# Performance work log

Measured on AMD Instinct MI355X. Metric: run time of the kernel, lower is better.

Reference implementation:

```python
import jax, jax.numpy as jnp
import numpy as np

B, T, D, K = 4, 4096, 1024, 64


def setup_inputs() -> dict:
    key = jax.random.key(0)
    k1, k2, k3, k4 = jax.random.split(key, 4)
    x = jax.random.normal(k1, (B, T, D), dtype=jnp.float32)
    Wq = jax.random.normal(k2, (D, K), dtype=jnp.float32) * (D ** -0.5)
    Wk = jax.random.normal(k3, (D, K), dtype=jnp.float32) * (D ** -0.5)
    Wv = jax.random.normal(k4, (D, D), dtype=jnp.float32) * (D ** -0.5)
    return {"x": x, "Wq": Wq, "Wk": Wk, "Wv": Wv}


def reference(x, Wq, Wk, Wv):
    # x: (B,T,D); single-head causal self-attention with value dim = D
    Bx, Tx, Dx = x.shape
    head_size = Wq.shape[-1]
    q = jnp.einsum('btd,dk->btk', x, Wq)  # (B,T,K)
    k = jnp.einsum('btd,dk->btk', x, Wk)  # (B,T,K)
    v = jnp.einsum('btd,de->bte', x, Wv)  # (B,T,D)
    scores = jnp.einsum('bqk,bsk->bqs', q, k) * (head_size ** -0.5)  # (B,T,T)
    causal = jnp.tril(jnp.ones((Tx, Tx), dtype=bool))
    scores = jnp.where(causal[None, :, :], scores, -jnp.inf)
    attn = jax.nn.softmax(scores, axis=-1)
    return jnp.einsum('bqs,bsd->bqd', attn, v)  # (B,T,D)
```

## Files before the change

kernel.cpp:

```cpp
#include <hip/hip_runtime.h>
#include <hip/hip_bf16.h>

typedef __attribute__((ext_vector_type(8))) short bf16x8;
typedef __attribute__((ext_vector_type(4))) float f32x4;
typedef unsigned short u16;

#define MFMA16(a, b, c) __builtin_amdgcn_mfma_f32_16x16x32_bf16((a), (b), (c), 0, 0, 0)
#define GLLDS(gp, lp)                                                                  \
  __builtin_amdgcn_global_load_lds((const __attribute__((address_space(1))) unsigned int*)(gp), \
                                   (__attribute__((address_space(3))) unsigned int*)(lp), 16, 0, 0)

__device__ __forceinline__ u16 f2b(float f) {
  union { float f; unsigned u; } x; x.f = f;
  return (u16)((x.u + 0x7FFFu + ((x.u >> 16) & 1u)) >> 16);
}
__device__ __forceinline__ u16 f2b_hw(float f) {
  union { __hip_bfloat16 h; u16 u; } c;
  c.h = __float2bfloat16(f);
  return c.u;
}

__global__ __launch_bounds__(256) void k_cvt(const float* __restrict__ in,
                                             u16* __restrict__ out, int n4) {
  int i = blockIdx.x * 256 + threadIdx.x;
  if (i >= n4) return;
  float4 v = ((const float4*)in)[i];
  u16 a = f2b(v.x), b = f2b(v.y), c = f2b(v.z), d = f2b(v.w);
  ((uint2*)out)[i] = make_uint2((unsigned)a | ((unsigned)b << 16),
                                (unsigned)c | ((unsigned)d << 16));
}

__global__ __launch_bounds__(256) void k_packT(const float* __restrict__ in,
                                               u16* __restrict__ out, int R, int C) {
  __shared__ float t[32][33];
  int r0 = blockIdx.x * 32, c0 = blockIdx.y * 32;
  int cx = threadIdx.x & 31, ry = threadIdx.x >> 5;
#pragma unroll
  for (int k = 0; k < 4; k++)
    t[ry + k * 8][cx] = in[(size_t)(r0 + ry + k * 8) * C + c0 + cx];
  __syncthreads();
#pragma unroll
  for (int k = 0; k < 4; k++)
    out[(size_t)(c0 + ry + k * 8) * R + r0 + cx] = f2b(t[cx][ry + k * 8]);
}

__global__ __launch_bounds__(256) void k_gemm_qk(const u16* __restrict__ xb,
                                                 const u16* __restrict__ wqt,
                                                 const u16* __restrict__ wkt,
                                                 u16* __restrict__ q, u16* __restrict__ kk) {
  int row0 = blockIdx.x * 64;
  int tid = threadIdx.x, w = tid >> 6, l = tid & 63, l15 = l & 15, lg = l >> 4;
  const u16* wt = (w < 2) ? wqt : wkt;
  int nbase = (w & 1) * 32;
  f32x4 acc[4][2];
#pragma unroll
  for (int mt = 0; mt < 4; mt++)
#pragma unroll
    for (int nt = 0; nt < 2; nt++) acc[mt][nt] = (f32x4){0.f, 0.f, 0.f, 0.f};

  for (int k0 = 0; k0 < 1024; k0 += 32) {
    bf16x8 bfr[2], afr[4];
#pragma unroll
    for (int nt = 0; nt < 2; nt++)
      bfr[nt] = *(const bf16x8*)&wt[(size_t)(nbase + nt * 16 + l15) * 1024 + k0 + lg * 8];
#pragma unroll
    for (int mt = 0; mt < 4; mt++)
      afr[mt] = *(const bf16x8*)&xb[(size_t)(row0 + mt * 16 + l15) * 1024 + k0 + lg * 8];
#pragma unroll
    for (int mt = 0; mt < 4; mt++)
#pragma unroll
      for (int nt = 0; nt < 2; nt++) acc[mt][nt] = MFMA16(afr[mt], bfr[nt], acc[mt][nt]);
  }
  if (w < 2) {
#pragma unroll
    for (int mt = 0; mt < 4; mt++)
#pragma unroll
      for (int nt = 0; nt < 2; nt++)
#pragma unroll
        for (int j = 0; j < 4; j++)
          q[(size_t)(row0 + mt * 16 + lg * 4 + j) * 64 + nbase + nt * 16 + l15] =
              f2b(acc[mt][nt][j] * 0.125f);
  } else {
#pragma unroll
    for (int mt = 0; mt < 4; mt++)
#pragma unroll
      for (int nt = 0; nt < 2; nt++)
#pragma unroll
        for (int j = 0; j < 4; j++) {
          int row = row0 + mt * 16 + lg * 4 + j;
          int c = (nbase + nt * 16 + l15) * 2;
          size_t off = (size_t)(row >> 6) * 8192 + (row & 63) * 128 + (c ^ ((row & 7) << 4));
          *(u16*)((char*)kk + off) = f2b(acc[mt][nt][j]);
        }
  }
}

__global__ __launch_bounds__(256) void k_gemm_v(const u16* __restrict__ xb,
                                                const u16* __restrict__ wvt,
                                                u16* __restrict__ vT) {
  int b = blockIdx.z;
  int d0 = blockIdx.y * 128;
  int s0 = blockIdx.x * 128;
  int tid = threadIdx.x, w = tid >> 6, l = tid & 63, l15 = l & 15, lg = l >> 4;
  int wd = (w & 1) * 64, wsn = (w >> 1) * 64;
  __shared__ __align__(16) char lds[32768];

  const u16* arow = wvt + (size_t)d0 * 1024;
  const u16* brow = xb + (size_t)(b * 4096 + s0) * 1024;

  auto stage = [&](int buf, int k0) {
    char* La = lds + buf * 16384;
    char* Lb = La + 8192;
#pragma unroll
    for (int i = 0; i < 2; i++) {
      int row = w * 32 + i * 16 + (l >> 2), kq = (l & 3) * 8;
      GLLDS(&arow[(size_t)row * 1024 + k0 + kq], La + (w * 2 + i) * 1024);
      GLLDS(&brow[(size_t)row * 1024 + k0 + kq], Lb + (w * 2 + i) * 1024);
    }
  };

  f32x4 acc[4][4];
#pragma unroll
  for (int mt = 0; mt < 4; mt++)
#pragma unroll
    for (int nt = 0; nt < 4; nt++) acc[mt][nt] = (f32x4){0.f, 0.f, 0.f, 0.f};

  stage(0, 0);
  __syncthreads();
  int buf = 0;
  for (int k = 0; k < 32; k++) {
    if (k < 31) stage(buf ^ 1, (k + 1) * 32);
    const char* La = lds + buf * 16384;
    const char* Lb = La + 8192;
    bf16x8 afr[4], bfr[4];
#pragma unroll
    for (int mt = 0; mt < 4; mt++)
      afr[mt] = *(const bf16x8*)(La + (wd + mt * 16 + l15) * 64 + lg * 16);
#pragma unroll
    for (int nt = 0; nt < 4; nt++)
      bfr[nt] = *(const bf16x8*)(Lb + (wsn + nt * 16 + l15) * 64 + lg * 16);
    __builtin_amdgcn_s_setprio(1);
#pragma unroll
    for (int mt = 0; mt < 4; mt++)
#pragma unroll
      for (int nt = 0; nt < 4; nt++) acc[mt][nt] = MFMA16(afr[mt], bfr[nt], acc[mt][nt]);
    __builtin_amdgcn_s_setprio(0);
    __syncthreads();
    buf ^= 1;
  }
#pragma unroll
  for (int mt = 0; mt < 4; mt++)
#pragma unroll
    for (int nt = 0; nt < 4; nt++)
#pragma unroll
      for (int j = 0; j < 4; j++) {
        int d = d0 + wd + mt * 16 + lg * 4 + j;
        int s = s0 + wsn + nt * 16 + l15;
        size_t off = ((size_t)(b * 64 + (s >> 6)) * 8 + (d >> 7)) * 16384 + (d & 127) * 128 +
                     (((s & 63) * 2) ^ ((d & 7) << 4));
        *(u16*)((char*)vT + off) = f2b(acc[mt][nt][j]);
      }
}

__global__ __launch_bounds__(512, 2) void k_attn(const u16* __restrict__ qw,
                                                 const u16* __restrict__ kws,
                                                 const u16* __restrict__ vts,
                                                 float* __restrict__ out) {
  int p = blockIdx.x, cpair = blockIdx.y, b = blockIdx.z;
  int tid = threadIdx.x, w = tid >> 6, l = tid & 63, l15 = l & 15, lg = l >> 4;
  int sw = (l15 & 7) << 4;
  size_t tokb = (size_t)b * 4096;

  __shared__ __align__(16) char lds[98816];
  char* Pb = lds + 81920;
  float* scb = (float*)(lds + 98304);

  const short ob = (short)0x3F80;
  const bf16x8 ones = {ob, ob, ob, ob, ob, ob, ob, ob};

  auto stage = [&](int t, int bufi) {
    const char* kb = (const char*)kws + (size_t)(b * 64 + t) * 8192;
    const char* vb = (const char*)vts + ((size_t)(b * 64 + t) * 8 + cpair * 2) * 16384;
    char* lk = lds + bufi * 8192;
    char* lv = lds + 16384 + bufi * 32768;
#pragma unroll
    for (int i = 0; i < 5; i++) {
      int s = w * 5 + i;
      if (s < 8) GLLDS(kb + s * 1024 + l * 16, lk + s * 1024);
      else       GLLDS(vb + (s - 8) * 1024 + l * 16, lv + (s - 8) * 1024);
    }
  };

  auto run_phase = [&](int Q0) {
    int ntb = (Q0 >> 6) + 2;
    int qsA = Q0 + w * 16;
    int qA = qsA + l15;
    int qsB = Q0 + (w & 3) * 32;
    int dhalf = w >> 2;

    bf16x8 qf[2];
#pragma unroll
    for (int ks = 0; ks < 2; ks++)
      qf[ks] = *(const bf16x8*)&qw[(tokb + qA) * 64 + ks * 32 + lg * 8];

    f32x4 acc[8][2], accl[2];
    float mrow = -1e30f;
#pragma unroll
    for (int mt = 0; mt < 8; mt++)
#pragma unroll
      for (int qt = 0; qt < 2; qt++) acc[mt][qt] = (f32x4){0.f, 0.f, 0.f, 0.f};
    accl[0] = (f32x4){0.f, 0.f, 0.f, 0.f};
    accl[1] = (f32x4){0.f, 0.f, 0.f, 0.f};

    stage(0, 0);
    __syncthreads();
    int buf = 0;
    for (int t = 0; t < ntb; t++) {
      int s0 = t * 64;
      if (t + 1 < ntb) stage(t + 1, buf ^ 1);
      if (s0 < qsA + 16) {
        const char* Kb = lds + buf * 8192;
        f32x4 sfr[4];
        __builtin_amdgcn_s_setprio(1);
#pragma unroll
        for (int nt = 0; nt < 4; nt++) {
          const char* kr = Kb + (nt * 16 + l15) * 128;
          bf16x8 kf0 = *(const bf16x8*)(kr + ((lg * 16) ^ sw));
          bf16x8 kf1 = *(const bf16x8*)(kr + ((64 + lg * 16) ^ sw));
          f32x4 z = (f32x4){0.f, 0.f, 0.f, 0.f};
          z = MFMA16(kf0, qf[0], z);
          sfr[nt] = MFMA16(kf1, qf[1], z);
        }
        __builtin_amdgcn_s_setprio(0);
        if (s0 + 63 > qsA) {
#pragma unroll
          for (int nt = 0; nt < 4; nt++)
#pragma unroll
            for (int j = 0; j < 4; j++)
              if (s0 + nt * 16 + lg * 4 + j > qA) sfr[nt][j] = -1e30f;
        }
        float pm = fmaxf(fmaxf(fmaxf(sfr[0][0], sfr[0][1]), fmaxf(sfr[0][2], sfr[0][3])),
                         fmaxf(fmaxf(sfr[1][0], sfr[1][1]), fmaxf(sfr[1][2], sfr[1][3])));
        pm = fmaxf(pm, fmaxf(fmaxf(fmaxf(sfr[2][0], sfr[2][1]), fmaxf(sfr[2][2], sfr[2][3])),
                             fmaxf(fmaxf(sfr[3][0], sfr[3][1]), fmaxf(sfr[3][2], sfr[3][3]))));
        pm = fmaxf(pm, __shfl_xor(pm, 16));
        pm = fmaxf(pm, __shfl_xor(pm, 32));
        float sc = 1.0f;
        if (__any(pm > mrow + 8.0f)) {
          float mn = fmaxf(mrow, pm);
          sc = __expf(mrow - mn);
          mrow = mn;
        }
        int rq = w * 16 + l15;
        scb[rq] = sc;
        int rbase = rq * 128, sx = (rq & 7) << 4;
#pragma unroll
        for (int nt = 0; nt < 4; nt++) {
          unsigned lo = (unsigned)f2b_hw(__expf(sfr[nt][0] - mrow)) |
                        ((unsigned)f2b_hw(__expf(sfr[nt][1] - mrow)) << 16);
          unsigned hi = (unsigned)f2b_hw(__expf(sfr[nt][2] - mrow)) |
                        ((unsigned)f2b_hw(__expf(sfr[nt][3] - mrow)) << 16);
          int addr = (rbase + (nt * 16 + lg * 4) * 2) ^ sx;
          *(uint2*)(Pb + addr) = make_uint2(lo, hi);
        }
      }
      __syncthreads();
      const char* Vb = lds + 16384 + buf * 32768 + dhalf * 16384;
#pragma unroll
      for (int qt = 0; qt < 2; qt++) {
        if (s0 < qsB + qt * 16 + 16) {
          float sq = scb[(w & 3) * 32 + qt * 16 + l15];
          if (!__all(sq == 1.0f)) {
#pragma unroll
            for (int mt = 0; mt < 8; mt++) acc[mt][qt] *= sq;
            accl[qt] *= sq;
          }
          int R = (w & 3) * 32 + qt * 16 + l15;
          int rx = (R & 7) << 4;
          bf16x8 pf0 = *(const bf16x8*)(Pb + ((R * 128 + lg * 16) ^ rx));
          bf16x8 pf1 = *(const bf16x8*)(Pb + ((R * 128 + 64 + lg * 16) ^ rx));
          __builtin_amdgcn_s_setprio(1);
          accl[qt] = MFMA16(ones, pf0, accl[qt]);
          accl[qt] = MFMA16(ones, pf1, accl[qt]);
#pragma unroll
          for (int mt = 0; mt < 8; mt++) {
            const char* vr = Vb + (mt * 16 + l15) * 128;
            bf16x8 va0 = *(const bf16x8*)(vr + ((lg * 16) ^ sw));
            bf16x8 va1 = *(const bf16x8*)(vr + ((64 + lg * 16) ^ sw));
            acc[mt][qt] = MFMA16(va0, pf0, acc[mt][qt]);
            acc[mt][qt] = MFMA16(va1, pf1, acc[mt][qt]);
          }
          __builtin_amdgcn_s_setprio(0);
        }
      }
      __syncthreads();
      buf ^= 1;
    }
#pragma unroll
    for (int qt = 0; qt < 2; qt++) {
      float linv = 1.0f / accl[qt][0];
#pragma unroll
      for (int mt = 0; mt < 8; mt++) {
        f32x4 v = acc[mt][qt] * linv;
        size_t o = (tokb + qsB + qt * 16 + l15) * 1024 + cpair * 256 + dhalf * 128 +
                   mt * 16 + lg * 4;
        *(f32x4*)&out[o] = v;
      }
    }
  };

  run_phase(p * 128);
  run_phase((31 - p) * 128);
}

extern "C" void kernel_launch(void* const* d_in, const int* in_sizes, int n_in,
                              void* d_out, int out_size, void* d_ws, size_t ws_size,
                              hipStream_t stream) {
  const float* x  = (const float*)d_in[0];
  const float* Wq = (const float*)d_in[1];
  const float* Wk = (const float*)d_in[2];
  const float* Wv = (const float*)d_in[3];
  float* out = (float*)d_out;
  char* ws = (char*)d_ws;
  u16* xb  = (u16*)(ws);
  u16* qw  = (u16*)(ws + 33554432);
  u16* kw  = (u16*)(ws + 35651584);
  u16* vT  = (u16*)(ws + 37748736);
  u16* wqt = (u16*)(ws + 71303168);
  u16* wkt = (u16*)(ws + 71434240);
  u16* wvt = (u16*)(ws + 71565312);

  k_cvt<<<16384, 256, 0, stream>>>(x, xb, 4194304);
  k_packT<<<dim3(32, 2), 256, 0, stream>>>(Wq, wqt, 1024, 64);
  k_packT<<<dim3(32, 2), 256, 0, stream>>>(Wk, wkt, 1024, 64);
  k_packT<<<dim3(32, 32), 256, 0, stream>>>(Wv, wvt, 1024, 1024);
  k_gemm_qk<<<256, 256, 0, stream>>>(xb, wqt, wkt, qw, kw);
  k_gemm_v<<<dim3(32, 8, 4), 256, 0, stream>>>(xb, wvt, vT);
  k_attn<<<dim3(16, 4, 4), 512, 0, stream>>>(qw, kw, vT, out);
}
```

Measured before the change: 237.5 us.

## Merge PV query-tile loops to share V fragments and use finer-grained barriers

The two query sub-tiles of the PV stage are now processed together. Each V fragment loaded from LDS feeds both accumulators, which halves V LDS reads, and an inactive first sub-tile is handled by zeroed P fragments instead of a branch. The full __syncthreads calls are replaced with explicit s_waitcnt plus s_barrier: only LDS counters are waited on mid-iteration, and global loads are drained only at the end of each iteration. The change risks extra MFMAs on masked diagonal tiles and depends on the hand-placed waitcnt being correct for the global_load_lds async copies.

```diff
diff --git a/kernel.cpp b/kernel.cpp
--- a/kernel.cpp
+++ b/kernel.cpp
@@ -177,6 +177,7 @@
 
   const short ob = (short)0x3F80;
   const bf16x8 ones = {ob, ob, ob, ob, ob, ob, ob, ob};
+  const bf16x8 zf = {0, 0, 0, 0, 0, 0, 0, 0};
 
   auto stage = [&](int t, int bufi) {
     const char* kb = (const char*)kws + (size_t)(b * 64 + t) * 8192;
@@ -213,7 +214,9 @@
     accl[1] = (f32x4){0.f, 0.f, 0.f, 0.f};
 
     stage(0, 0);
-    __syncthreads();
+    asm volatile("s_waitcnt vmcnt(0)" ::: "memory");
+    __builtin_amdgcn_s_barrier();
+    asm volatile("" ::: "memory");
     int buf = 0;
     for (int t = 0; t < ntb; t++) {
       int s0 = t * 64;
@@ -264,36 +267,60 @@
           *(uint2*)(Pb + addr) = make_uint2(lo, hi);
         }
       }
-      __syncthreads();
-      const char* Vb = lds + 16384 + buf * 32768 + dhalf * 16384;
-#pragma unroll
-      for (int qt = 0; qt < 2; qt++) {
-        if (s0 < qsB + qt * 16 + 16) {
-          float sq = scb[(w & 3) * 32 + qt * 16 + l15];
-          if (!__all(sq == 1.0f)) {
-#pragma unroll
-            for (int mt = 0; mt < 8; mt++) acc[mt][qt] *= sq;
-            accl[qt] *= sq;
+      asm volatile("s_waitcnt lgkmcnt(0)" ::: "memory");
+      __builtin_amdgcn_s_barrier();
+      asm volatile("" ::: "memory");
+      if (s0 < qsB + 32) {
+        const char* Vb = lds + 16384 + buf * 32768 + dhalf * 16384;
+        bool act0 = s0 < qsB + 16;
+        int R0 = (w & 3) * 32 + l15;
+        if (act0) {
+          float sq0 = scb[R0];
+          if (!__all(sq0 == 1.0f)) {
+#pragma unroll
+            for (int mt = 0; mt < 8; mt++) acc[mt][0] *= sq0;
+            accl[0] *= sq0;
           }
-          int R = (w & 3) * 32 + qt * 16 + l15;
-          int rx = (R & 7) << 4;
-          bf16x8 pf0 = *(const bf16x8*)(Pb + ((R * 128 + lg * 16) ^ rx));
-          bf16x8 pf1 = *(const bf16x8*)(Pb + ((R * 128 + 64 + lg * 16) ^ rx));
-          __builtin_amdgcn_s_setprio(1);
-          accl[qt] = MFMA16(ones, pf0, accl[qt]);
-          accl[qt] = MFMA16(ones, pf1, accl[qt]);
-#pragma unroll
-          for (int mt = 0; mt < 8; mt++) {
-            const char* vr = Vb + (mt * 16 + l15) * 128;
-            bf16x8 va0 = *(const bf16x8*)(vr + ((lg * 16) ^ sw));
-            bf16x8 va1 = *(const bf16x8*)(vr + ((64 + lg * 16) ^ sw));
-            acc[mt][qt] = MFMA16(va0, pf0, acc[mt][qt]);
-            acc[mt][qt] = MFMA16(va1, pf1, acc[mt][qt]);
+        }
+        {
+          float sq1 = scb[R0 + 16];
+          if (!__all(sq1 == 1.0f)) {
+#pragma unroll
+            for (int mt = 0; mt < 8; mt++) acc[mt][1] *= sq1;
+            accl[1] *= sq1;
           }
-          __builtin_amdgcn_s_setprio(0);
-        }
+        }
+        bf16x8 pf00 = zf, pf01 = zf, pf10, pf11;
+        if (act0) {
+          int rx = (R0 & 7) << 4;
+          pf00 = *(const bf16x8*)(Pb + ((R0 * 128 + lg * 16) ^ rx));
+          pf01 = *(const bf16x8*)(Pb + ((R0 * 128 + 64 + lg * 16) ^ rx));
+        }
+        {
+          int R1 = R0 + 16, rx = (R1 & 7) << 4;
+          pf10 = *(const bf16x8*)(Pb + ((R1 * 128 + lg * 16) ^ rx));
+          pf11 = *(const bf16x8*)(Pb + ((R1 * 128 + 64 + lg * 16) ^ rx));
+        }
+        __builtin_amdgcn_s_setprio(1);
+        accl[0] = MFMA16(ones, pf00, accl[0]);
+        accl[0] = MFMA16(ones, pf01, accl[0]);
+        accl[1] = MFMA16(ones, pf10, accl[1]);
+        accl[1] = MFMA16(ones, pf11, accl[1]);
+#pragma unroll
+        for (int mt = 0; mt < 8; mt++) {
+          const char* vr = Vb + (mt * 16 + l15) * 128;
+          bf16x8 va0 = *(const bf16x8*)(vr + ((lg * 16) ^ sw));
+          bf16x8 va1 = *(const bf16x8*)(vr + ((64 + lg * 16) ^ sw));
+          acc[mt][0] = MFMA16(va0, pf00, acc[mt][0]);
+          acc[mt][0] = MFMA16(va1, pf01, acc[mt][0]);
+          acc[mt][1] = MFMA16(va0, pf10, acc[mt][1]);
+          acc[mt][1] = MFMA16(va1, pf11, acc[mt][1]);
+        }
+        __builtin_amdgcn_s_setprio(0);
       }
-      __syncthreads();
+      asm volatile("s_waitcnt vmcnt(0)" ::: "memory");
+      __builtin_amdgcn_s_barrier();
+      asm volatile("" ::: "memory");
       buf ^= 1;
     }
 #pragma unroll
```

After: 252.6 us. 6.3% more time.

## Warp-specialize attention: score warps feed PV warps via double-buffered P

Applied to the files above, without the earlier changes.

Splits the eight waves of the attention block into four producer waves that compute QK scores, softmax and write P, and four consumer waves that run P·V one tile behind, using a double-buffered P and scale buffer in LDS. This lets the QK and softmax stage overlap the PV MFMA stage instead of serialising them within every wave. Each consumer wave now holds 4x8 accumulators, which raises register pressure. The grid is also flattened and remapped so blocks sharing a batch and column pair land on the same XCD for L2 reuse, and K and V staging is split across waves.

```diff
diff --git a/kernel.cpp b/kernel.cpp
--- a/kernel.cpp
+++ b/kernel.cpp
@@ -14,10 +14,10 @@
   union { float f; unsigned u; } x; x.f = f;
   return (u16)((x.u + 0x7FFFu + ((x.u >> 16) & 1u)) >> 16);
 }
-__device__ __forceinline__ u16 f2b_hw(float f) {
+__device__ __forceinline__ unsigned f2b_hw(float f) {
   union { __hip_bfloat16 h; u16 u; } c;
   c.h = __float2bfloat16(f);
-  return c.u;
+  return (unsigned)c.u;
 }
 
 __global__ __launch_bounds__(256) void k_cvt(const float* __restrict__ in,
@@ -166,145 +166,196 @@
                                                  const u16* __restrict__ kws,
                                                  const u16* __restrict__ vts,
                                                  float* __restrict__ out) {
-  int p = blockIdx.x, cpair = blockIdx.y, b = blockIdx.z;
+  int bid = blockIdx.x;
+  int xcd = bid & 7, rest = bid >> 3;
+  int p = rest & 15, hi = rest >> 4;
+  int g = xcd + 8 * hi;
+  int cpair = g & 3, b = g >> 2;
   int tid = threadIdx.x, w = tid >> 6, l = tid & 63, l15 = l & 15, lg = l >> 4;
   int sw = (l15 & 7) << 4;
   size_t tokb = (size_t)b * 4096;
-
-  __shared__ __align__(16) char lds[98816];
-  char* Pb = lds + 81920;
-  float* scb = (float*)(lds + 98304);
+  bool isA = w < 4;
+  int wq = w & 3;
+  int qpos = wq & 1, dhalf = wq >> 1;
+
+  __shared__ __align__(16) char lds[115712];
 
   const short ob = (short)0x3F80;
   const bf16x8 ones = {ob, ob, ob, ob, ob, ob, ob, ob};
 
-  auto stage = [&](int t, int bufi) {
+  auto stageV = [&](int t, int bufi) {
+    const char* vb = (const char*)vts + ((size_t)(b * 64 + t) * 8 + cpair * 2) * 16384;
+    char* lv = lds + 16384 + bufi * 32768;
+#pragma unroll
+    for (int i = 0; i < 4; i++) GLLDS(vb + (w * 4 + i) * 1024 + l * 16, lv + (w * 4 + i) * 1024);
+  };
+  auto stageK = [&](int t, int bufi) {
     const char* kb = (const char*)kws + (size_t)(b * 64 + t) * 8192;
-    const char* vb = (const char*)vts + ((size_t)(b * 64 + t) * 8 + cpair * 2) * 16384;
-    char* lk = lds + bufi * 8192;
-    char* lv = lds + 16384 + bufi * 32768;
-#pragma unroll
-    for (int i = 0; i < 5; i++) {
-      int s = w * 5 + i;
-      if (s < 8) GLLDS(kb + s * 1024 + l * 16, lk + s * 1024);
-      else       GLLDS(vb + (s - 8) * 1024 + l * 16, lv + (s - 8) * 1024);
-    }
+    GLLDS(kb + w * 1024 + l * 16, lds + bufi * 8192 + w * 1024);
   };
 
   auto run_phase = [&](int Q0) {
     int ntb = (Q0 >> 6) + 2;
-    int qsA = Q0 + w * 16;
-    int qA = qsA + l15;
-    int qsB = Q0 + (w & 3) * 32;
-    int dhalf = w >> 2;
-
-    bf16x8 qf[2];
-#pragma unroll
-    for (int ks = 0; ks < 2; ks++)
-      qf[ks] = *(const bf16x8*)&qw[(tokb + qA) * 64 + ks * 32 + lg * 8];
-
-    f32x4 acc[8][2], accl[2];
-    float mrow = -1e30f;
+    int qsA = Q0 + wq * 32;
+    int qsB = Q0 + qpos * 64;
+
+    bf16x8 qf[2][2];
+    if (isA) {
+#pragma unroll
+      for (int cb = 0; cb < 2; cb++)
+#pragma unroll
+        for (int ks = 0; ks < 2; ks++)
+          qf[cb][ks] =
+              *(const bf16x8*)&qw[(tokb + qsA + cb * 16 + l15) * 64 + ks * 32 + lg * 8];
+    }
+
+    f32x4 acc[8][4], accl[4];
+    float mrow[2];
 #pragma unroll
     for (int mt = 0; mt < 8; mt++)
 #pragma unroll
-      for (int qt = 0; qt < 2; qt++) acc[mt][qt] = (f32x4){0.f, 0.f, 0.f, 0.f};
-    accl[0] = (f32x4){0.f, 0.f, 0.f, 0.f};
-    accl[1] = (f32x4){0.f, 0.f, 0.f, 0.f};
-
-    stage(0, 0);
+      for (int qt = 0; qt < 4; qt++) acc[mt][qt] = (f32x4){0.f, 0.f, 0.f, 0.f};
+#pragma unroll
+    for (int qt = 0; qt < 4; qt++) accl[qt] = (f32x4){0.f, 0.f, 0.f, 0.f};
+    mrow[0] = mrow[1] = -1e30f;
+
+    stageK(0, 0);
     __syncthreads();
-    int buf = 0;
-    for (int t = 0; t < ntb; t++) {
-      int s0 = t * 64;
-      if (t + 1 < ntb) stage(t + 1, buf ^ 1);
-      if (s0 < qsA + 16) {
-        const char* Kb = lds + buf * 8192;
-        f32x4 sfr[4];
-        __builtin_amdgcn_s_setprio(1);
-#pragma unroll
-        for (int nt = 0; nt < 4; nt++) {
-          const char* kr = Kb + (nt * 16 + l15) * 128;
-          bf16x8 kf0 = *(const bf16x8*)(kr + ((lg * 16) ^ sw));
-          bf16x8 kf1 = *(const bf16x8*)(kr + ((64 + lg * 16) ^ sw));
-          f32x4 z = (f32x4){0.f, 0.f, 0.f, 0.f};
-          z = MFMA16(kf0, qf[0], z);
-          sfr[nt] = MFMA16(kf1, qf[1], z);
+    for (int t = 0; t <= ntb; t++) {
+      if (t < ntb) stageV(t, t & 1);
+      if (t + 1 < ntb) stageK(t + 1, (t + 1) & 1);
+      if (isA) {
+        int s0 = t * 64;
+        if (t < ntb && s0 < qsA + 32) {
+          const char* Kb = lds + (t & 1) * 8192;
+          char* Pw = lds + 81920 + (t & 1) * 16384;
+          float* scw = (float*)(lds + 114688) + (t & 1) * 128;
+          f32x4 sfr[2][4];
+          __builtin_amdgcn_s_setprio(1);
+#pragma unroll
+          for (int nt = 0; nt < 4; nt++) {
+            const char* kr = Kb + (nt * 16 + l15) * 128;
+            bf16x8 kf0 = *(const bf16x8*)(kr + ((lg * 16) ^ sw));
+            bf16x8 kf1 = *(const bf16x8*)(kr + ((64 + lg * 16) ^ sw));
+#pragma unroll
+            for (int cb = 0; cb < 2; cb++) {
+              f32x4 z = (f32x4){0.f, 0.f, 0.f, 0.f};
+              z = MFMA16(kf0, qf[cb][0], z);
+              sfr[cb][nt] = MFMA16(kf1, qf[cb][1], z);
+            }
+          }
+          __builtin_amdgcn_s_setprio(0);
+          if (s0 + 63 > qsA) {
+#pragma unroll
+            for (int cb = 0; cb < 2; cb++) {
+              int qv = qsA + cb * 16 + l15;
+#pragma unroll
+              for (int nt = 0; nt < 4; nt++)
+#pragma unroll
+                for (int j = 0; j < 4; j++)
+                  if (s0 + nt * 16 + lg * 4 + j > qv) sfr[cb][nt][j] = -1e30f;
+            }
+          }
+          float pm[2];
+          int need = 0;
+#pragma unroll
+          for (int cb = 0; cb < 2; cb++) {
+            pm[cb] = fmaxf(fmaxf(fmaxf(sfr[cb][0][0], sfr[cb][0][1]),
+                                 fmaxf(sfr[cb][0][2], sfr[cb][0][3])),
+                           fmaxf(fmaxf(sfr[cb][1][0], sfr[cb][1][1]),
+                                 fmaxf(sfr[cb][1][2], sfr[cb][1][3])));
+            pm[cb] = fmaxf(pm[cb], fmaxf(fmaxf(fmaxf(sfr[cb][2][0], sfr[cb][2][1]),
+                                               fmaxf(sfr[cb][2][2], sfr[cb][2][3])),
+                                         fmaxf(fmaxf(sfr[cb][3][0], sfr[cb][3][1]),
+                                               fmaxf(sfr[cb][3][2], sfr[cb][3][3]))));
+            pm[cb] = fmaxf(pm[cb], __shfl_xor(pm[cb], 16));
+            pm[cb] = fmaxf(pm[cb], __shfl_xor(pm[cb], 32));
+            need |= (pm[cb] > mrow[cb] + 8.0f);
+          }
+          float scv[2] = {1.0f, 1.0f};
+          if (__any(need)) {
+#pragma unroll
+            for (int cb = 0; cb < 2; cb++) {
+              float mn = fmaxf(mrow[cb], pm[cb]);
+              scv[cb] = __expf(mrow[cb] - mn);
+              mrow[cb] = mn;
+            }
+          }
+#pragma unroll
+          for (int cb = 0; cb < 2; cb++) {
+            int rq = wq * 32 + cb * 16 + l15;
+            scw[rq] = scv[cb];
+            int rbase = rq * 128, sx = (rq & 7) << 4;
+#pragma unroll
+            for (int nt = 0; nt < 4; nt++) {
+              unsigned lo = f2b_hw(__expf(sfr[cb][nt][0] - mrow[cb])) |
+                            (f2b_hw(__expf(sfr[cb][nt][1] - mrow[cb])) << 16);
+              unsigned hi2 = f2b_hw(__expf(sfr[cb][nt][2] - mrow[cb])) |
+                             (f2b_hw(__expf(sfr[cb][nt][3] - mrow[cb])) << 16);
+              int addr = (rbase + (nt * 16 + lg * 4) * 2) ^ sx;
+              *(uint2*)(Pw + addr) = make_uint2(lo, hi2);
+            }
+          }
         }
-        __builtin_amdgcn_s_setprio(0);
-        if (s0 + 63 > qsA) {
-#pragma unroll
-          for (int nt = 0; nt < 4; nt++)
-#pragma unroll
-            for (int j = 0; j < 4; j++)
-              if (s0 + nt * 16 + lg * 4 + j > qA) sfr[nt][j] = -1e30f;
-        }
-        float pm = fmaxf(fmaxf(fmaxf(sfr[0][0], sfr[0][1]), fmaxf(sfr[0][2], sfr[0][3])),
-                         fmaxf(fmaxf(sfr[1][0], sfr[1][1]), fmaxf(sfr[1][2], sfr[1][3])));
-        pm = fmaxf(pm, fmaxf(fmaxf(fmaxf(sfr[2][0], sfr[2][1]), fmaxf(sfr[2][2], sfr[2][3])),
-                             fmaxf(fmaxf(sfr[3][0], sfr[3][1]), fmaxf(sfr[3][2], sfr[3][3]))));
-        pm = fmaxf(pm, __shfl_xor(pm, 16));
-        pm = fmaxf(pm, __shfl_xor(pm, 32));
-        float sc = 1.0f;
-        if (__any(pm > mrow + 8.0f)) {
-          float mn = fmaxf(mrow, pm);
-          sc = __expf(mrow - mn);
-          mrow = mn;
-        }
-        int rq = w * 16 + l15;
-        scb[rq] = sc;
-        int rbase = rq * 128, sx = (rq & 7) << 4;
-#pragma unroll
-        for (int nt = 0; nt < 4; nt++) {
-          unsigned lo = (unsigned)f2b_hw(__expf(sfr[nt][0] - mrow)) |
-                        ((unsigned)f2b_hw(__expf(sfr[nt][1] - mrow)) << 16);
-          unsigned hi = (unsigned)f2b_hw(__expf(sfr[nt][2] - mrow)) |
-                        ((unsigned)f2b_hw(__expf(sfr[nt][3] - mrow)) << 16);
-          int addr = (rbase + (nt * 16 + lg * 4) * 2) ^ sx;
-          *(uint2*)(Pb + addr) = make_uint2(lo, hi);
-        }
-      }
-      __syncthreads();
-      const char* Vb = lds + 16384 + buf * 32768 + dhalf * 16384;
-#pragma unroll
-      for (int qt = 0; qt < 2; qt++) {
-        if (s0 < qsB + qt * 16 + 16) {
-          float sq = scb[(w & 3) * 32 + qt * 16 + l15];
-          if (!__all(sq == 1.0f)) {
-#pragma unroll
-            for (int mt = 0; mt < 8; mt++) acc[mt][qt] *= sq;
-            accl[qt] *= sq;
-          }
-          int R = (w & 3) * 32 + qt * 16 + l15;
-          int rx = (R & 7) << 4;
-          bf16x8 pf0 = *(const bf16x8*)(Pb + ((R * 128 + lg * 16) ^ rx));
-          bf16x8 pf1 = *(const bf16x8*)(Pb + ((R * 128 + 64 + lg * 16) ^ rx));
+      } else if (t >= 1) {
+        int tb = t - 1, s0 = tb * 64;
+        int qlo = (s0 - qsB) >> 4;
+        if (qlo < 0) qlo = 0;
+        if (qlo < 4) {
+          int bi = tb & 1;
+          const char* Pb = lds + 81920 + bi * 16384;
+          const float* scb = (const float*)(lds + 114688) + bi * 128;
+          const char* Vb = lds + 16384 + bi * 32768 + dhalf * 16384;
+          bf16x8 pf[4][2];
+#pragma unroll
+          for (int qt = 0; qt < 4; qt++)
+            if (qt >= qlo) {
+              int R = qpos * 64 + qt * 16 + l15;
+              float sq = scb[R];
+              if (!__all(sq == 1.0f)) {
+#pragma unroll
+                for (int mt = 0; mt < 8; mt++) acc[mt][qt] *= sq;
+                accl[qt] *= sq;
+              }
+              int rx = (R & 7) << 4;
+              pf[qt][0] = *(const bf16x8*)(Pb + ((R * 128 + lg * 16) ^ rx));
+              pf[qt][1] = *(const bf16x8*)(Pb + ((R * 128 + 64 + lg * 16) ^ rx));
+            }
           __builtin_amdgcn_s_setprio(1);
-          accl[qt] = MFMA16(ones, pf0, accl[qt]);
-          accl[qt] = MFMA16(ones, pf1, accl[qt]);
+#pragma unroll
+          for (int qt = 0; qt < 4; qt++)
+            if (qt >= qlo) {
+              accl[qt] = MFMA16(ones, pf[qt][0], accl[qt]);
+              accl[qt] = MFMA16(ones, pf[qt][1], accl[qt]);
+            }
 #pragma unroll
           for (int mt = 0; mt < 8; mt++) {
             const char* vr = Vb + (mt * 16 + l15) * 128;
             bf16x8 va0 = *(const bf16x8*)(vr + ((lg * 16) ^ sw));
             bf16x8 va1 = *(const bf16x8*)(vr + ((64 + lg * 16) ^ sw));
-            acc[mt][qt] = MFMA16(va0, pf0, acc[mt][qt]);
-            acc[mt][qt] = MFMA16(va1, pf1, acc[mt][qt]);
+#pragma unroll
+            for (int qt = 0; qt < 4; qt++)
+              if (qt >= qlo) {
+                acc[mt][qt] = MFMA16(va0, pf[qt][0], acc[mt][qt]);
+                acc[mt][qt] = MFMA16(va1, pf[qt][1], acc[mt][qt]);
+              }
           }
           __builtin_amdgcn_s_setprio(0);
         }
       }
       __syncthreads();
-      buf ^= 1;
     }
-#pragma unroll
-    for (int qt = 0; qt < 2; qt++) {
-      float linv = 1.0f / accl[qt][0];
-#pragma unroll
-      for (int mt = 0; mt < 8; mt++) {
-        f32x4 v = acc[mt][qt] * linv;
-        size_t o = (tokb + qsB + qt * 16 + l15) * 1024 + cpair * 256 + dhalf * 128 +
-                   mt * 16 + lg * 4;
-        *(f32x4*)&out[o] = v;
+    if (!isA) {
+#pragma unroll
+      for (int qt = 0; qt < 4; qt++) {
+        float linv = 1.0f / accl[qt][0];
+#pragma unroll
+        for (int mt = 0; mt < 8; mt++) {
+          f32x4 v = acc[mt][qt] * linv;
+          size_t o = (tokb + qsB + qt * 16 + l15) * 1024 + cpair * 256 + dhalf * 128 +
+                     mt * 16 + lg * 4;
+          *(f32x4*)&out[o] = v;
+        }
       }
     }
   };
@@ -336,5 +387,5 @@
   k_packT<<<dim3(32, 32), 256, 0, stream>>>(Wv, wvt, 1024, 1024);
   k_gemm_qk<<<256, 256, 0, stream>>>(xb, wqt, wkt, qw, kw);
   k_gemm_v<<<dim3(32, 8, 4), 256, 0, stream>>>(xb, wvt, vT);
-  k_attn<<<dim3(16, 4, 4), 512, 0, stream>>>(qw, kw, vT, out);
-}
+  k_attn<<<256, 512, 0, stream>>>(qw, kw, vT, out);
+}
```

Result: slower. 317.8 us (+33.8%).
